# Performance work log

Measured on AMD Instinct MI355X. Metric: run time of the kernel, lower is better.

Reference implementation:

```python
import jax, jax.numpy as jnp
import numpy as np

B, N, C = 2, 2048, 1024
H = 16
HD = C // H  # 64


def setup_inputs() -> dict:
    key = jax.random.key(0)
    ks = jax.random.split(key, 6)
    x = jax.random.normal(ks[0], (B, N, C), dtype=jnp.float32)
    # realistic rotary angles
    inv_freq = 1.0 / (10000.0 ** (np.arange(0, HD, 2, dtype=np.float32) / HD))
    t = np.arange(N, dtype=np.float32)
    freqs = np.outer(t, inv_freq)                      # [N, HD/2]
    emb = np.concatenate([freqs, freqs], axis=-1)      # [N, HD]
    cos = jnp.asarray(np.cos(emb), dtype=jnp.float32)
    sin = jnp.asarray(np.sin(emb), dtype=jnp.float32)
    qkv_w = jax.random.normal(ks[1], (3 * C, C), dtype=jnp.float32) * (1.0 / np.sqrt(C))
    proj_w = jax.random.normal(ks[2], (C, C), dtype=jnp.float32) * (1.0 / np.sqrt(C))
    proj_b = jnp.zeros((C,), dtype=jnp.float32)
    return {"x": x, "cos": cos, "sin": sin, "qkv_w": qkv_w, "proj_w": proj_w, "proj_b": proj_b}


def _apply_rope(x, cos, sin):
    # x: [B, H, N, HD]; cos/sin: [N, HD] (broadcast over B, H)
    x1, x2 = jnp.split(x, 2, axis=-1)
    rotated = jnp.concatenate([-x2, x1], axis=-1)
    return x * cos + rotated * sin


def reference(x, cos, sin, qkv_w, proj_w, proj_b):
    b, n, c = x.shape
    scale = (c // H) ** (-0.5)
    qkv = jnp.einsum('bnc,dc->bnd', x, qkv_w)          # [B, N, 3C]
    qkv = qkv.reshape(b, n, 3, H, HD).transpose(2, 0, 3, 1, 4)  # [3, B, H, N, HD]
    q, k, v = qkv[0], qkv[1], qkv[2]
    q = _apply_rope(q, cos, sin)
    k = _apply_rope(k, cos, sin)
    attn = jnp.einsum('bhid,bhjd->bhij', q, k) * scale  # [B, H, N, N]
    attn = jax.nn.softmax(attn, axis=-1)
    out = jnp.einsum('bhij,bhjd->bhid', attn, v)        # [B, H, N, HD]
    out = out.transpose(0, 2, 1, 3).reshape(b, n, c)    # [B, N, C]
    return jnp.einsum('bnc,dc->bnd', out, proj_w) + proj_b
```

## Files before the change

kernel.cpp:

```cpp
#include <hip/hip_runtime.h>
#include <stdint.h>

typedef __bf16 bf16;
typedef bf16 bf16x8 __attribute__((ext_vector_type(8)));
typedef float f32x4 __attribute__((ext_vector_type(4)));
typedef float f32x16 __attribute__((ext_vector_type(16)));
typedef unsigned short u16x8 __attribute__((ext_vector_type(8)));
typedef unsigned short u16x4 __attribute__((ext_vector_type(4)));

__device__ __forceinline__ unsigned short f2bfu(float f) {
    union { bf16 h; unsigned short u; } x;
    x.h = (bf16)f;
    return x.u;
}
__device__ __forceinline__ float bfu2f(unsigned short u) {
    union { unsigned int i; float f; } x;
    x.i = ((unsigned int)u) << 16;
    return x.f;
}
__device__ __forceinline__ unsigned int pack2bf(float a, float b) {
    union { bf16 h[2]; unsigned int u; } x;
    x.h[0] = (bf16)a; x.h[1] = (bf16)b;
    return x.u;
}
__device__ __forceinline__ void pl32_swap(unsigned int &a, unsigned int &b) {
    asm volatile("v_permlane32_swap_b32 %0, %1" : "+v"(a), "+v"(b));
}

__device__ __forceinline__ void gld_lds16(const void* g, void* l) {
    __builtin_amdgcn_global_load_lds(
        (const __attribute__((address_space(1))) unsigned int*)(uintptr_t)g,
        (__attribute__((address_space(3))) unsigned int*)(unsigned int)(uintptr_t)l,
        16, 0, 0);
}

__global__ void cast_bf16_kernel(const float* __restrict__ in,
                                 unsigned short* __restrict__ out, int n8) {
    int i = blockIdx.x * blockDim.x + threadIdx.x;
    if (i >= n8) return;
    const f32x4* p = (const f32x4*)(in + (size_t)i * 8);
    f32x4 a = p[0], b = p[1];
    u16x8 o;
    o[0]=f2bfu(a[0]); o[1]=f2bfu(a[1]); o[2]=f2bfu(a[2]); o[3]=f2bfu(a[3]);
    o[4]=f2bfu(b[0]); o[5]=f2bfu(b[1]); o[6]=f2bfu(b[2]); o[7]=f2bfu(b[3]);
    *(u16x8*)(out + (size_t)i * 8) = o;
}

__global__ void rope_kernel(unsigned short* __restrict__ qkv,
                            const float* __restrict__ cosp,
                            const float* __restrict__ sinp) {
    int tid = blockIdx.x * blockDim.x + threadIdx.x;
    int i8  = tid & 3;
    int h   = (tid >> 2) & 15;
    int sel = (tid >> 6) & 1;
    int n   = (tid >> 7) & 2047;
    int b   = tid >> 18;
    size_t base = ((size_t)(b*2048 + n))*3072 + sel*1024 + h*64 + i8*8;
    u16x8 x1 = *(u16x8*)(qkv + base);
    u16x8 x2 = *(u16x8*)(qkv + base + 32);
    const f32x4* cp = (const f32x4*)(cosp + n*64 + i8*8);
    const f32x4* sp = (const f32x4*)(sinp + n*64 + i8*8);
    f32x4 c0 = cp[0], c1 = cp[1], s0 = sp[0], s1 = sp[1];
    float scale = sel ? 1.0f : (0.125f * 1.44269504088896f);
    u16x8 o1, o2;
#pragma unroll
    for (int j = 0; j < 8; j++) {
        float cc = (j < 4) ? c0[j] : c1[j-4];
        float ss = (j < 4) ? s0[j] : s1[j-4];
        float a = bfu2f(x1[j]), d = bfu2f(x2[j]);
        o1[j] = f2bfu((a*cc - d*ss) * scale);
        o2[j] = f2bfu((d*cc + a*ss) * scale);
    }
    *(u16x8*)(qkv + base)      = o1;
    *(u16x8*)(qkv + base + 32) = o2;
}

template<int OUT_F32>
__global__ __launch_bounds__(256, 2) void gemm_bt(
    const unsigned short* __restrict__ A, const unsigned short* __restrict__ B,
    void* __restrict__ Cp, const float* __restrict__ bias,
    int M, int N, int K)
{
    __shared__ __align__(16) unsigned short As[2][128*32];
    __shared__ __align__(16) unsigned short Bs[2][128*32];
    int nwg  = gridDim.x * gridDim.y;
    int orig = blockIdx.y * gridDim.x + blockIdx.x;
    int qq = nwg >> 3, rr = nwg & 7;
    int xcd = orig & 7, idx = orig >> 3;
    int wg = (xcd < rr) ? (xcd*(qq+1) + idx) : (rr*(qq+1) + (xcd-rr)*qq + idx);
    int bx = wg % gridDim.x, by = wg / gridDim.x;
    int m0 = by * 128, n0 = bx * 128;
    int t = threadIdx.x;
    int w = t >> 6, l = t & 63;
    int c = l & 15, g = l >> 4;
    int wm = (w >> 1) * 64, wn = (w & 1) * 64;

    auto stage = [&](int kt, int bsel) {
#pragma unroll
        for (int r2 = 0; r2 < 2; ++r2) {
            int xb = w*2048 + r2*1024;
            int x  = xb + l*16;
            int row  = x >> 6;
            int colu = (x & 63) >> 1;
            int k0 = kt << 5;
            gld_lds16(A + (size_t)(m0+row)*K + k0 + colu, (void*)(As[bsel] + (xb >> 1)));
            gld_lds16(B + (size_t)(n0+row)*K + k0 + colu, (void*)(Bs[bsel] + (xb >> 1)));
        }
    };

    f32x4 acc[4][4];
#pragma unroll
    for (int i = 0; i < 4; i++)
#pragma unroll
        for (int j = 0; j < 4; j++) acc[i][j] = f32x4{0.f,0.f,0.f,0.f};

    int nkt = K >> 5;
    stage(0, 0);
    int cur = 0;
    for (int kt = 0; kt < nkt; ++kt) {
        __syncthreads();
        if (kt + 1 < nkt) stage(kt + 1, cur ^ 1);
        const unsigned short* Ab = As[cur] + wm*32;
        const unsigned short* Bb = Bs[cur] + wn*32;
        bf16x8 af[4], bfr[4];
#pragma unroll
        for (int i = 0; i < 4; i++) af[i]  = *(const bf16x8*)(Ab + (i*16+c)*32 + g*8);
#pragma unroll
        for (int i = 0; i < 4; i++) bfr[i] = *(const bf16x8*)(Bb + (i*16+c)*32 + g*8);
#pragma unroll
        for (int i = 0; i < 4; i++)
#pragma unroll
            for (int j = 0; j < 4; j++)
                acc[i][j] = __builtin_amdgcn_mfma_f32_16x16x32_bf16(af[i], bfr[j], acc[i][j], 0, 0, 0);
        cur ^= 1;
    }
#pragma unroll
    for (int i = 0; i < 4; i++)
#pragma unroll
        for (int j = 0; j < 4; j++)
#pragma unroll
            for (int e = 0; e < 4; e++) {
                int row = m0 + wm + i*16 + g*4 + e;
                int col = n0 + wn + j*16 + c;
                float v = acc[i][j][e];
                if (bias) v += bias[col];
                if (OUT_F32) ((float*)Cp)[(size_t)row*N + col] = v;
                else ((unsigned short*)Cp)[(size_t)row*N + col] = f2bfu(v);
            }
}

__global__ __launch_bounds__(256, 2) void attn_kernel(
    const unsigned short* __restrict__ qkv, unsigned short* __restrict__ outp)
{
    __shared__ __align__(16) unsigned short Ks[2][64*64];
    __shared__ __align__(16) unsigned short Vt[2][64*64];
    int bh = blockIdx.y;
    int b = bh >> 4, h = bh & 15;
    int q0 = blockIdx.x << 7;
    int t = threadIdx.x;
    int w = t >> 6, l = t & 63;
    int q = l & 31, hi = l >> 5;
    int qw = q0 + w*32;
    size_t bh_base = ((size_t)b*2048)*3072 + (size_t)h*64;

    auto stageK = [&](int kv0, int bsel) {
#pragma unroll
        for (int r2 = 0; r2 < 2; ++r2) {
            int xb = w*2048 + r2*1024;
            int x  = xb + l*16;
            int row  = x >> 7;
            int scolb = (x & 127) ^ ((row & 7) << 4);
            gld_lds16(qkv + bh_base + 1024 + (size_t)(kv0 + row)*3072 + (scolb >> 1),
                      (void*)(Ks[bsel] + (xb >> 1)));
        }
    };
    auto loadV = [&](int kv0, u16x8 &v0, u16x8 &v1) {
        int p  = t >> 3;
        int hb = (t & 7) << 3;
        const unsigned short* src = qkv + bh_base + 2048 + (size_t)(kv0 + 2*p)*3072 + hb;
        v0 = *(const u16x8*)src;
        v1 = *(const u16x8*)(src + 3072);
    };
    auto writeV = [&](const u16x8 &v0, const u16x8 &v1, int bsel) {
        int p  = t >> 3;
        int hb = (t & 7) << 3;
#pragma unroll
        for (int e = 0; e < 8; e++) {
            int hd = hb + e;
            int colb = (4*p) ^ ((((hd) ^ (hd >> 3)) & 7) << 4);
            *(unsigned int*)((char*)Vt[bsel] + hd*128 + colb) =
                (unsigned int)v0[e] | ((unsigned int)v1[e] << 16);
        }
    };

    bf16x8 qf[4];
#pragma unroll
    for (int dc = 0; dc < 4; dc++)
        qf[dc] = *(const bf16x8*)(qkv + bh_base + (size_t)(qw + q)*3072 + dc*16 + hi*8);

    f32x16 oacc[2];
#pragma unroll
    for (int e = 0; e < 16; e++) { oacc[0][e] = 0.f; oacc[1][e] = 0.f; }
    float lsum = 0.f;

    u16x8 vc0, vc1, vn0, vn1;
    stageK(0, 0);
    loadV(0, vc0, vc1);
    int cur = 0;

    for (int kvt = 0; kvt < 32; ++kvt) {
        writeV(vc0, vc1, cur);
        __syncthreads();
        if (kvt < 31) {
            int kv0n = (kvt + 1) << 6;
            stageK(kv0n, cur ^ 1);
            loadV(kv0n, vn0, vn1);
        }
        const char* ksb = (const char*)Ks[cur];
        const char* vtb = (const char*)Vt[cur];

#pragma unroll
        for (int sblk = 0; sblk < 2; ++sblk) {
            f32x16 st;
#pragma unroll
            for (int e = 0; e < 16; e++) st[e] = 0.f;
            int krow = sblk*32 + q;
            int ksw = (krow & 7) << 4;
#pragma unroll
            for (int dc = 0; dc < 4; ++dc) {
                bf16x8 kf = *(const bf16x8*)(ksb + krow*128 + ((dc*32 + hi*16) ^ ksw));
                st = __builtin_amdgcn_mfma_f32_32x32x16_bf16(kf, qf[dc], st, 0, 0, 0);
            }
            unsigned int wds[8];
#pragma unroll
            for (int m = 0; m < 8; m++) {
                float p0 = __builtin_amdgcn_exp2f(st[2*m]);
                float p1 = __builtin_amdgcn_exp2f(st[2*m+1]);
                lsum += p0 + p1;
                wds[m] = pack2bf(p0, p1);
            }
#pragma unroll
            for (int half = 0; half < 2; ++half) {
                unsigned int a0 = wds[half*4 + 0], b0 = wds[half*4 + 2];
                unsigned int a1 = wds[half*4 + 1], b1 = wds[half*4 + 3];
                pl32_swap(a0, b0);
                pl32_swap(a1, b1);
                union { unsigned int u[4]; bf16x8 v; } pf;
                pf.u[0] = a0; pf.u[1] = a1; pf.u[2] = b0; pf.u[3] = b1;
                int kc = sblk*2 + half;
#pragma unroll
                for (int hdblk = 0; hdblk < 2; ++hdblk) {
                    int hd = hdblk*32 + q;
                    int vsw = ((hd ^ (hd >> 3)) & 7) << 4;
                    bf16x8 vf = *(const bf16x8*)(vtb + hd*128 + ((kc*32 + hi*16) ^ vsw));
                    oacc[hdblk] = __builtin_amdgcn_mfma_f32_32x32x16_bf16(vf, pf.v, oacc[hdblk], 0, 0, 0);
                }
            }
        }
        vc0 = vn0; vc1 = vn1;
        cur ^= 1;
    }
    float ltot = lsum + __shfl_xor(lsum, 32, 64);
    float rinv = 1.0f / ltot;
    size_t orow = (size_t)(b*2048 + qw + q) * 1024 + h*64;
#pragma unroll
    for (int hdblk = 0; hdblk < 2; ++hdblk)
#pragma unroll
        for (int quad = 0; quad < 4; ++quad) {
            u16x4 o4;
#pragma unroll
            for (int j = 0; j < 4; j++)
                o4[j] = f2bfu(oacc[hdblk][quad*4 + j] * rinv);
            *(u16x4*)(outp + orow + hdblk*32 + quad*8 + hi*4) = o4;
        }
}

extern "C" void kernel_launch(void* const* d_in, const int* in_sizes, int n_in,
                              void* d_out, int out_size, void* d_ws, size_t ws_size,
                              hipStream_t stream) {
    const float* x      = (const float*)d_in[0];
    const float* cosp   = (const float*)d_in[1];
    const float* sinp   = (const float*)d_in[2];
    const float* qkv_w  = (const float*)d_in[3];
    const float* proj_w = (const float*)d_in[4];
    const float* proj_b = (const float*)d_in[5];

    char* ws = (char*)d_ws;
    unsigned short* xb     = (unsigned short*)(ws);
    unsigned short* wqkvb  = (unsigned short*)(ws + (size_t)(8u << 20));
    unsigned short* wprojb = (unsigned short*)(ws + (size_t)(14u << 20));
    unsigned short* qkvb   = (unsigned short*)(ws + (size_t)(16u << 20));
    unsigned short* attno  = xb;

    cast_bf16_kernel<<<2048, 256, 0, stream>>>(x, xb, 524288);
    cast_bf16_kernel<<<1536, 256, 0, stream>>>(qkv_w, wqkvb, 393216);
    cast_bf16_kernel<<<512, 256, 0, stream>>>(proj_w, wprojb, 131072);

    gemm_bt<0><<<dim3(24, 32), 256, 0, stream>>>(xb, wqkvb, (void*)qkvb, nullptr, 4096, 3072, 1024);
    rope_kernel<<<2048, 256, 0, stream>>>(qkvb, cosp, sinp);
    attn_kernel<<<dim3(16, 32), 256, 0, stream>>>(qkvb, attno);
    gemm_bt<1><<<dim3(8, 32), 256, 0, stream>>>(attno, wprojb, d_out, proj_b, 4096, 1024, 1024);
}
```

Baseline: 134.9 us.

## Add 256x256-tile triple-buffered 8-wave GEMM for QKV projection

Replaces the 128x128 double-buffered QKV GEMM with a new kernel using 256x256 output tiles, 512 threads (8 waves each computing 128x64), and a three-stage LDS ring filled with direct global-to-LDS loads plus an XOR swizzle. Larger tiles raise arithmetic intensity per LDS byte, and the deeper pipeline with split MFMA phases and s_setprio aims to overlap loads with compute. In exchange it uses 96KB of dynamic shared memory and launches only 192 workgroups, which is fewer than the GPU's CU count, so occupancy and load balance may suffer. The epilogue writes scalar bf16 stores, which may not coalesce well.

```diff
diff --git a/kernel.cpp b/kernel.cpp
--- a/kernel.cpp
+++ b/kernel.cpp
@@ -73,6 +73,98 @@
     }
     *(u16x8*)(qkv + base)      = o1;
     *(u16x8*)(qkv + base + 32) = o2;
+}
+
+__global__ __launch_bounds__(512, 2) void gemm_qkv8(
+    const unsigned short* __restrict__ A, const unsigned short* __restrict__ B,
+    unsigned short* __restrict__ C, int M, int N, int K)
+{
+    extern __shared__ char smem[];
+    int nwgx = gridDim.x;
+    int nwg  = nwgx * gridDim.y;
+    int orig = blockIdx.y * nwgx + blockIdx.x;
+    int cpx  = nwg >> 3;
+    int wg   = (orig & 7) * cpx + (orig >> 3);
+    int bx = wg % nwgx, by = wg / nwgx;
+    int m0 = by << 8, n0 = bx << 8;
+    int t  = threadIdx.x;
+    int wv = t >> 6, l = t & 63;
+    int fr = l & 15, fq = l >> 4;
+    int wm = (wv >> 2) << 7;
+    int wn = (wv & 3) << 6;
+    int aswz = (fr & 3) << 4;
+
+    auto stage = [&](int kt, int bsel) {
+        int k0 = kt << 5;
+        char* base = smem + (bsel << 15);
+#pragma unroll
+        for (int j = 0; j < 2; ++j) {
+            int y   = (j << 13) + t * 16;
+            int ly  = y ^ (((y >> 6) & 3) << 4);
+            int row = ly >> 6;
+            int colu = (ly & 63) >> 1;
+            gld_lds16(A + (size_t)(m0 + row) * K + k0 + colu,
+                      base + ((j << 13) + (wv << 10)));
+            gld_lds16(B + (size_t)(n0 + row) * K + k0 + colu,
+                      base + 16384 + ((j << 13) + (wv << 10)));
+        }
+    };
+
+    f32x4 acc[8][4];
+#pragma unroll
+    for (int m = 0; m < 8; ++m)
+#pragma unroll
+        for (int n = 0; n < 4; ++n) acc[m][n] = f32x4{0.f, 0.f, 0.f, 0.f};
+
+    stage(0, 0);
+    stage(1, 1);
+    int cb = 0;
+    for (int kt = 0; kt < 32; ++kt) {
+        if (kt < 31) asm volatile("s_waitcnt vmcnt(4)" ::: "memory");
+        else         asm volatile("s_waitcnt vmcnt(0)" ::: "memory");
+        __builtin_amdgcn_s_barrier();
+        if (kt + 2 < 32) {
+            int sb = cb - 1; if (sb < 0) sb = 2;
+            stage(kt + 2, sb);
+        }
+        const char* base = smem + (cb << 15);
+        const char* Ab = base + ((wm + fr) << 6) + ((fq * 16) ^ aswz);
+        const char* Bb = base + 16384 + ((wn + fr) << 6) + ((fq * 16) ^ aswz);
+        bf16x8 bfr[4], af[4];
+#pragma unroll
+        for (int n = 0; n < 4; ++n) bfr[n] = *(const bf16x8*)(Bb + (n << 10));
+#pragma unroll
+        for (int m = 0; m < 4; ++m) af[m]  = *(const bf16x8*)(Ab + (m << 10));
+        __builtin_amdgcn_s_barrier();
+        __builtin_amdgcn_s_setprio(1);
+#pragma unroll
+        for (int m = 0; m < 4; ++m)
+#pragma unroll
+            for (int n = 0; n < 4; ++n)
+                acc[m][n] = __builtin_amdgcn_mfma_f32_16x16x32_bf16(af[m], bfr[n], acc[m][n], 0, 0, 0);
+        __builtin_amdgcn_s_setprio(0);
+#pragma unroll
+        for (int m = 0; m < 4; ++m) af[m] = *(const bf16x8*)(Ab + ((m + 4) << 10));
+        __builtin_amdgcn_s_barrier();
+        __builtin_amdgcn_s_setprio(1);
+#pragma unroll
+        for (int m = 0; m < 4; ++m)
+#pragma unroll
+            for (int n = 0; n < 4; ++n)
+                acc[m + 4][n] = __builtin_amdgcn_mfma_f32_16x16x32_bf16(af[m], bfr[n], acc[m + 4][n], 0, 0, 0);
+        __builtin_amdgcn_s_setprio(0);
+        cb = (cb == 2) ? 0 : cb + 1;
+    }
+#pragma unroll
+    for (int m = 0; m < 8; ++m)
+#pragma unroll
+        for (int n = 0; n < 4; ++n)
+#pragma unroll
+            for (int e = 0; e < 4; ++e) {
+                int row = m0 + wm + m * 16 + fq * 4 + e;
+                int col = n0 + wn + n * 16 + fr;
+                C[(size_t)row * N + col] = f2bfu(acc[m][n][e]);
+            }
 }
 
 template<int OUT_F32>
@@ -296,7 +388,9 @@
     cast_bf16_kernel<<<1536, 256, 0, stream>>>(qkv_w, wqkvb, 393216);
     cast_bf16_kernel<<<512, 256, 0, stream>>>(proj_w, wprojb, 131072);
 
-    gemm_bt<0><<<dim3(24, 32), 256, 0, stream>>>(xb, wqkvb, (void*)qkvb, nullptr, 4096, 3072, 1024);
+    hipFuncSetAttribute((const void*)gemm_qkv8,
+                        hipFuncAttributeMaxDynamicSharedMemorySize, 98304);
+    gemm_qkv8<<<dim3(12, 16), 512, 98304, stream>>>(xb, wqkvb, qkvb, 4096, 3072, 1024);
     rope_kernel<<<2048, 256, 0, stream>>>(qkvb, cosp, sinp);
     attn_kernel<<<dim3(16, 32), 256, 0, stream>>>(qkvb, attno);
     gemm_bt<1><<<dim3(8, 32), 256, 0, stream>>>(attno, wprojb, d_out, proj_b, 4096, 1024, 1024);
```

Measured after the change: 135.2 us. About the same (+0.2%).
